# Kernel tuning notes

Hardware: AMD Instinct MI355X
Metric: run time of the kernel (lower is better)

The kernel has to match this reference:

```python
import jax, jax.numpy as jnp
import numpy as np

DIM = 1024
HID = 1536  # int(1024 * 1.5)
K = 4       # conv kernel size
N, T = 4, 4096


def _mk_forget_base(h, a=0.001, b=0.1, lo=-4.323, hi=-9.0):
    x = np.log(np.expm1(np.linspace(a, b, h, dtype=np.float64)))
    x = (x - x.min()) / (x.max() - x.min())
    x = x * abs(hi - lo) + hi
    return jnp.asarray(x, dtype=jnp.float32)


def setup_inputs() -> dict:
    key = jax.random.key(0)
    ks = jax.random.split(key, 6)
    x = jax.random.normal(ks[0], (N, T, DIM), jnp.float32)
    Wi = jax.random.normal(ks[1], (2 * HID, DIM), jnp.float32) * DIM ** -0.5
    conv_w = jax.random.normal(ks[2], (HID, 1, K), jnp.float32) * K ** -0.5
    conv_b = jax.random.normal(ks[3], (HID,), jnp.float32) * 0.01
    Wg = jax.random.normal(ks[4], (2 * HID, HID), jnp.float32) * HID ** -0.5
    bg = jnp.zeros((2 * HID,), jnp.float32)
    forget_base = _mk_forget_base(HID)
    Wo = jax.random.normal(ks[5], (DIM, HID), jnp.float32) * HID ** -0.5
    return {"x": x, "Wi": Wi, "conv_w": conv_w, "conv_b": conv_b,
            "Wg": Wg, "bg": bg, "forget_base": forget_base, "Wo": Wo}


def reference(x, Wi, conv_w, conv_b, Wg, bg, forget_base, Wo):
    # input projection -> gate, x  (each [N,T,HID])
    gi = jnp.einsum('ntc,hc->nth', x, Wi)
    gate, u = jnp.split(gi, 2, axis=-1)
    # causal depthwise conv1d (torch pads k-1 both sides then slices [:T])
    u = jax.lax.conv_general_dilated(
        u.transpose(0, 2, 1),            # [N,HID,T]
        conv_w,                           # [HID,1,K]
        window_strides=(1,),
        padding=[(K - 1, 0)],
        dimension_numbers=('NCH', 'OIH', 'NCH'),
        feature_group_count=HID,
    ) + conv_b[None, :, None]
    u = u.transpose(0, 2, 1)              # [N,T,HID]
    # gates
    fg = jnp.einsum('nth,gh->ntg', u, Wg) + bg
    forget, inp = jnp.split(fg, 2, axis=-1)
    # RG-LRU decay: alpha = exp(-8 * softplus(forget_base) * sigmoid(forget))
    alpha = jnp.exp(-8.0 * jax.nn.softplus(forget_base) * jax.nn.sigmoid(forget))
    beta = jnp.sqrt(1.0 - alpha ** 2 + 1e-6)
    xt = beta * jax.nn.sigmoid(inp) * u
    # linear recurrence h_t = alpha_t * h_{t-1} + x_t
    def step(h, ax):
        a, xx = ax
        h = a * h + xx
        return h, h
    _, h = jax.lax.scan(step, jnp.zeros((x.shape[0], HID), x.dtype),
                        (alpha.transpose(1, 0, 2), xt.transpose(1, 0, 2)))
    h = h.transpose(1, 0, 2)              # [N,T,HID]
    # output projection with exact (erf) gelu gate, matching torch default
    return jnp.einsum('nth,ch->ntc', jax.nn.gelu(gate, approximate=False) * h, Wo)
```

## Files before the change

kernel.cpp:

```cpp
#include <hip/hip_runtime.h>

#define DIM 1024
#define HID 1536
#define TT 4096
#define NB 4
#define KCONV 4
#define MROWS (NB * TT)
#define NC 128
#define CH (TT / NC)
#define H8 (HID / 8)
#define H4 (HID / 4)
#define TC 16

typedef unsigned short u16;
typedef short bf16x8 __attribute__((ext_vector_type(8)));
typedef u16 u16x4 __attribute__((ext_vector_type(4)));
typedef float f32x4 __attribute__((ext_vector_type(4)));

__device__ __forceinline__ u16 f2bf(float f) {
  union { float f; unsigned u; } v; v.f = f;
  unsigned r = (v.u + 0x7fffu + ((v.u >> 16) & 1u)) >> 16;
  return (u16)r;
}
__device__ __forceinline__ float bf2f(u16 h) {
  union { unsigned u; float f; } v; v.u = ((unsigned)h) << 16;
  return v.f;
}
__device__ __forceinline__ float gelu_exact(float g) {
  return 0.5f * g * (1.0f + erff(g * 0.70710678118f));
}

__global__ void cvt_bf16(const float* __restrict__ in, u16* __restrict__ out, int n4) {
  int i = blockIdx.x * blockDim.x + threadIdx.x;
  if (i < n4) {
    float4 v = reinterpret_cast<const float4*>(in)[i];
    ushort4 o;
    o.x = f2bf(v.x); o.y = f2bf(v.y); o.z = f2bf(v.z); o.w = f2bf(v.w);
    reinterpret_cast<ushort4*>(out)[i] = o;
  }
}

#define AS1q __attribute__((address_space(1)))
#define AS3q __attribute__((address_space(3)))
__device__ __forceinline__ void glds16(const u16* g, u16* l) {
  __builtin_amdgcn_global_load_lds((const AS1q void*)g, (AS3q void*)l, 16, 0, 0);
}

#define BAR    asm volatile("s_barrier" ::: "memory")
#define WAITV4 asm volatile("s_waitcnt vmcnt(4)" ::: "memory")
#define WAITV0 asm volatile("s_waitcnt vmcnt(0)" ::: "memory")

template <int EPI>
__global__ __launch_bounds__(512, 2) void gemm256(
    const u16* __restrict__ A, const u16* __restrict__ B,
    float* __restrict__ C, u16* __restrict__ O0, u16* __restrict__ O1,
    int M, int Nn, int K, int gx) {
  __shared__ u16 LA[2][2][8192];
  __shared__ u16 LB[2][2][8192];
  const int tid = threadIdx.x;
  const int l = tid & 63;
  const int wid = tid >> 6;
  const int wr = wid >> 2;
  const int wc = wid & 3;

  const int bid = blockIdx.x;
  const int gm8 = (M >> 8) >> 3;
  const int xcd = bid & 7;
  const int idx = bid >> 3;
  const int mg  = idx / (4 * gx);
  const int rem = idx % (4 * gx);
  const int nn  = rem >> 2;
  const int mi  = rem & 3;
  const int tileM = (xcd * gm8 + mg * 4 + mi) * 256;
  const int tileN = nn * 256;

  const int lp = l ^ ((l & 32) >> 4);
  const int srow = lp >> 2;
  const int scol = (lp & 3) * 8;
  const int rdoff = ((l & 15) * 32 + (l >> 4) * 8) ^ ((l & 8) << 1);

  const u16* Abase = A + (size_t)(tileM + wid * 32 + srow) * K + scol;
  const u16* Bbase = B + (size_t)(tileN + wid * 32 + srow) * K + scol;

#define STAGE_A(c, kk, kt) { const u16* g_ = Abase + (size_t)(kt) * 64 + (kk) * 32; \
    glds16(g_, &LA[c][kk][wid * 1024]); glds16(g_ + 16 * (size_t)K, &LA[c][kk][wid * 1024 + 512]); }
#define STAGE_B(c, kk, kt) { const u16* g_ = Bbase + (size_t)(kt) * 64 + (kk) * 32; \
    glds16(g_, &LB[c][kk][wid * 1024]); glds16(g_ + 16 * (size_t)K, &LB[c][kk][wid * 1024 + 512]); }

  f32x4 acc[8][4] = {};
  bf16x8 a[8], b[4];

#define LDB4(c, kk) { _Pragma("unroll") for (int ni = 0; ni < 4; ni++) \
    b[ni] = *(const bf16x8*)&LB[c][kk][(wc * 4 + ni) * 512 + rdoff]; }
#define LDA8(c, kk) { _Pragma("unroll") for (int mi2 = 0; mi2 < 8; mi2++) \
    a[mi2] = *(const bf16x8*)&LA[c][kk][(wr * 8 + mi2) * 512 + rdoff]; }
#define MFMA32 { __builtin_amdgcn_s_setprio(1); \
    _Pragma("unroll") for (int mi2 = 0; mi2 < 8; mi2++) \
    _Pragma("unroll") for (int ni = 0; ni < 4; ni++) \
      acc[mi2][ni] = __builtin_amdgcn_mfma_f32_16x16x32_bf16(a[mi2], b[ni], acc[mi2][ni], 0, 0, 0); \
    __builtin_amdgcn_s_setprio(0); }

  STAGE_A(0, 0, 0); STAGE_B(0, 0, 0);
  STAGE_A(0, 1, 0); STAGE_B(0, 1, 0);
  STAGE_A(1, 0, 1); STAGE_B(1, 0, 1);
  WAITV4; BAR;

  const int NIT = K >> 7;
  for (int i = 0; i < NIT; i++) {
    const int kt = 2 * i;
    const bool nl = (i + 1 < NIT);
    LDB4(0, 0); LDA8(0, 0); STAGE_A(1, 1, kt + 1); STAGE_B(1, 1, kt + 1);
    BAR; MFMA32; BAR;
    LDB4(0, 1); LDA8(0, 1); if (nl) { STAGE_A(0, 0, kt + 2); STAGE_B(0, 0, kt + 2); }
    BAR; MFMA32; if (nl) { WAITV4; } else { WAITV0; } BAR;
    LDB4(1, 0); LDA8(1, 0); if (nl) { STAGE_A(0, 1, kt + 2); STAGE_B(0, 1, kt + 2); }
    BAR; MFMA32; BAR;
    LDB4(1, 1); LDA8(1, 1); if (nl) { STAGE_A(1, 0, kt + 3); STAGE_B(1, 0, kt + 3); }
    BAR; MFMA32; if (nl) { WAITV4; } else { WAITV0; } BAR;
  }

  const int r0 = tileM + wr * 128 + (l >> 4) * 4;
  const int c0 = tileN + wc * 64 + (l & 15);
  if (EPI == 0) {
#pragma unroll
    for (int ai = 0; ai < 8; ai++)
#pragma unroll
      for (int ni = 0; ni < 4; ni++)
#pragma unroll
        for (int r = 0; r < 4; r++)
          C[(size_t)(r0 + ai * 16 + r) * Nn + (c0 + ni * 16)] = acc[ai][ni][r];
  } else {
    const bool lo = (tileN < HID);
    u16* dst = lo ? O0 : O1;
    const int cb = lo ? 0 : HID;
#pragma unroll
    for (int ai = 0; ai < 8; ai++)
#pragma unroll
      for (int ni = 0; ni < 4; ni++)
#pragma unroll
        for (int r = 0; r < 4; r++) {
          float v = acc[ai][ni][r];
          if (EPI == 2 && lo) v = gelu_exact(v);
          dst[(size_t)(r0 + ai * 16 + r) * HID + (c0 + ni * 16 - cb)] = f2bf(v);
        }
  }
#undef STAGE_A
#undef STAGE_B
#undef LDB4
#undef LDA8
#undef MFMA32
}

__global__ void conv1d_k(const u16* __restrict__ u, const float* __restrict__ w,
                         const float* __restrict__ b, u16* __restrict__ uc) {
  int idx = blockIdx.x * blockDim.x + threadIdx.x;
  int hb = (idx % H8) * 8;
  int rc = idx / H8;
  int t0 = (rc % (TT / TC)) * TC;
  int n  = rc / (TT / TC);

  float wt[KCONV][8], bias[8];
#pragma unroll
  for (int j = 0; j < 8; j++) {
    float4 wj = reinterpret_cast<const float4*>(w)[hb + j];
    wt[0][j] = wj.x; wt[1][j] = wj.y; wt[2][j] = wj.z; wt[3][j] = wj.w;
    bias[j] = b[hb + j];
  }

  const u16* up = u + (size_t)n * TT * HID + hb;
  u16* op = uc + (size_t)n * TT * HID + hb;
  bf16x8 zero;
#pragma unroll
  for (int j = 0; j < 8; j++) zero[j] = 0;
  bf16x8 w0 = (t0 > 0) ? *(const bf16x8*)&up[(size_t)(t0 - 3) * HID] : zero;
  bf16x8 w1 = (t0 > 0) ? *(const bf16x8*)&up[(size_t)(t0 - 2) * HID] : zero;
  bf16x8 w2 = (t0 > 0) ? *(const bf16x8*)&up[(size_t)(t0 - 1) * HID] : zero;
#pragma unroll 4
  for (int t = t0; t < t0 + TC; t++) {
    bf16x8 cur = *(const bf16x8*)&up[(size_t)t * HID];
    bf16x8 o;
#pragma unroll
    for (int j = 0; j < 8; j++) {
      float a = bias[j];
      a += bf2f((u16)w0[j]) * wt[0][j];
      a += bf2f((u16)w1[j]) * wt[1][j];
      a += bf2f((u16)w2[j]) * wt[2][j];
      a += bf2f((u16)cur[j]) * wt[3][j];
      o[j] = (short)f2bf(a);
    }
    *(bf16x8*)&op[(size_t)t * HID] = o;
    w0 = w1; w1 = w2; w2 = cur;
  }
}

__global__ void scan_phase1(const u16* __restrict__ fbuf, const u16* __restrict__ ibuf,
                            const u16* __restrict__ ubuf, const float* __restrict__ fb,
                            const float* __restrict__ bg,
                            float* __restrict__ Ac, float* __restrict__ Bc) {
  int tid = blockIdx.x * blockDim.x + threadIdx.x;
  int hb = (tid % H4) * 4;
  int nc = tid / H4;
  int n = nc % NB;
  int c = nc / NB;
  f32x4 fbv = *reinterpret_cast<const f32x4*>(&fb[hb]);
  f32x4 bgf = *reinterpret_cast<const f32x4*>(&bg[hb]);
  f32x4 bgi = *reinterpret_cast<const f32x4*>(&bg[HID + hb]);
  float c8[4], ap[4] = {1.f, 1.f, 1.f, 1.f}, hl[4] = {0.f, 0.f, 0.f, 0.f};
#pragma unroll
  for (int j = 0; j < 4; j++) c8[j] = 8.0f * log1pf(expf(fbv[j]));
  size_t base = ((size_t)n * TT + (size_t)c * CH) * HID + hb;
  for (int t = 0; t < CH; t++) {
    size_t ix = base + (size_t)t * HID;
    u16x4 f4 = *reinterpret_cast<const u16x4*>(&fbuf[ix]);
    u16x4 i4 = *reinterpret_cast<const u16x4*>(&ibuf[ix]);
    u16x4 u4 = *reinterpret_cast<const u16x4*>(&ubuf[ix]);
#pragma unroll
    for (int j = 0; j < 4; j++) {
      float f = bf2f(f4[j]) + bgf[j];
      float sf = 1.0f / (1.0f + expf(-f));
      float al = expf(-c8[j] * sf);
      float be = sqrtf(1.0f - al * al + 1e-6f);
      float xi = bf2f(i4[j]) + bgi[j];
      float si = 1.0f / (1.0f + expf(-xi));
      float xt = be * si * bf2f(u4[j]);
      hl[j] = al * hl[j] + xt;
      ap[j] *= al;
    }
  }
  size_t ci = ((size_t)c * NB + n) * HID + hb;
  *reinterpret_cast<f32x4*>(&Ac[ci]) = f32x4{ap[0], ap[1], ap[2], ap[3]};
  *reinterpret_cast<f32x4*>(&Bc[ci]) = f32x4{hl[0], hl[1], hl[2], hl[3]};
}

__global__ void scan_phase2(const float* __restrict__ Ac, const float* __restrict__ Bc,
                            float* __restrict__ Carry) {
  int tid = blockIdx.x * blockDim.x + threadIdx.x;
  int h = tid % HID;
  int n = tid / HID;
  float carry = 0.f;
#pragma unroll 4
  for (int c = 0; c < NC; c++) {
    size_t ci = ((size_t)c * NB + n) * HID + h;
    Carry[ci] = carry;
    carry = Ac[ci] * carry + Bc[ci];
  }
}

__global__ void scan_phase3(const u16* __restrict__ fbuf, const u16* __restrict__ ibuf,
                            const u16* __restrict__ ubuf, const u16* __restrict__ gbuf,
                            const float* __restrict__ fb, const float* __restrict__ bg,
                            const float* __restrict__ Carry, u16* __restrict__ gh) {
  int tid = blockIdx.x * blockDim.x + threadIdx.x;
  int hb = (tid % H4) * 4;
  int nc = tid / H4;
  int n = nc % NB;
  int c = nc / NB;
  f32x4 fbv = *reinterpret_cast<const f32x4*>(&fb[hb]);
  f32x4 bgf = *reinterpret_cast<const f32x4*>(&bg[hb]);
  f32x4 bgi = *reinterpret_cast<const f32x4*>(&bg[HID + hb]);
  float c8[4], hc[4];
#pragma unroll
  for (int j = 0; j < 4; j++) c8[j] = 8.0f * log1pf(expf(fbv[j]));
  size_t ci = ((size_t)c * NB + n) * HID + hb;
  f32x4 cv = *reinterpret_cast<const f32x4*>(&Carry[ci]);
#pragma unroll
  for (int j = 0; j < 4; j++) hc[j] = cv[j];
  size_t base = ((size_t)n * TT + (size_t)c * CH) * HID + hb;
  for (int t = 0; t < CH; t++) {
    size_t ix = base + (size_t)t * HID;
    u16x4 f4 = *reinterpret_cast<const u16x4*>(&fbuf[ix]);
    u16x4 i4 = *reinterpret_cast<const u16x4*>(&ibuf[ix]);
    u16x4 u4 = *reinterpret_cast<const u16x4*>(&ubuf[ix]);
    u16x4 g4 = *reinterpret_cast<const u16x4*>(&gbuf[ix]);
    u16x4 o4;
#pragma unroll
    for (int j = 0; j < 4; j++) {
      float f = bf2f(f4[j]) + bgf[j];
      float sf = 1.0f / (1.0f + expf(-f));
      float al = expf(-c8[j] * sf);
      float be = sqrtf(1.0f - al * al + 1e-6f);
      float xi = bf2f(i4[j]) + bgi[j];
      float si = 1.0f / (1.0f + expf(-xi));
      float xt = be * si * bf2f(u4[j]);
      hc[j] = al * hc[j] + xt;
      o4[j] = f2bf(bf2f(g4[j]) * hc[j]);
    }
    *reinterpret_cast<u16x4*>(&gh[ix]) = o4;
  }
}

extern "C" void kernel_launch(void* const* d_in, const int* in_sizes, int n_in,
                              void* d_out, int out_size, void* d_ws, size_t ws_size,
                              hipStream_t stream) {
  const float* x  = (const float*)d_in[0];
  const float* Wi = (const float*)d_in[1];
  const float* cw = (const float*)d_in[2];
  const float* cb = (const float*)d_in[3];
  const float* Wg = (const float*)d_in[4];
  const float* bg = (const float*)d_in[5];
  const float* fb = (const float*)d_in[6];
  const float* Wo = (const float*)d_in[7];
  float* out = (float*)d_out;

  const size_t SZ_XBF = (size_t)MROWS * DIM * 2;
  const size_t SZ_WI  = (size_t)2 * HID * DIM * 2;
  const size_t SZ_WG  = (size_t)2 * HID * HID * 2;
  const size_t SZ_WO  = (size_t)DIM * HID * 2;
  const size_t SZ_ACT = (size_t)MROWS * HID * 2;
  const size_t REQUIRED = SZ_XBF + SZ_WI + SZ_WG + SZ_WO + 4 * SZ_ACT;
  if (ws_size < REQUIRED) return;

  char* p = (char*)d_ws;
  auto alloc = [&](size_t bytes) { char* q = p; p += bytes; return q; };
  u16* x_bf   = (u16*)alloc(SZ_XBF);
  u16* Wi_bf  = (u16*)alloc(SZ_WI);
  u16* Wg_bf  = (u16*)alloc(SZ_WG);
  u16* Wo_bf  = (u16*)alloc(SZ_WO);
  u16* u_bf   = (u16*)alloc(SZ_ACT);
  u16* uc_bf  = (u16*)alloc(SZ_ACT);
  u16* fg0_bf = (u16*)alloc(SZ_ACT);
  u16* fg1_bf = (u16*)alloc(SZ_ACT);
  u16* gh_bf  = u_bf;

  u16* gate_bf = (u16*)d_out;
  float* Ac    = (float*)((char*)d_out + SZ_ACT);
  float* Bc    = Ac + (size_t)NC * NB * HID;
  float* Carry = Bc + (size_t)NC * NB * HID;

  cvt_bf16<<<(MROWS * DIM / 4) / 256, 256, 0, stream>>>(x, x_bf, MROWS * DIM / 4);
  cvt_bf16<<<(2 * HID * DIM / 4) / 256, 256, 0, stream>>>(Wi, Wi_bf, 2 * HID * DIM / 4);
  cvt_bf16<<<(2 * HID * HID / 4) / 256, 256, 0, stream>>>(Wg, Wg_bf, 2 * HID * HID / 4);
  cvt_bf16<<<(DIM * HID / 4) / 256, 256, 0, stream>>>(Wo, Wo_bf, DIM * HID / 4);

  gemm256<2><<<(2 * HID / 256) * (MROWS / 256), 512, 0, stream>>>(
      x_bf, Wi_bf, nullptr, gate_bf, u_bf, MROWS, 2 * HID, DIM, 2 * HID / 256);
  conv1d_k<<<(NB * (TT / TC) * H8) / 256, 256, 0, stream>>>(u_bf, cw, cb, uc_bf);
  gemm256<1><<<(2 * HID / 256) * (MROWS / 256), 512, 0, stream>>>(
      uc_bf, Wg_bf, nullptr, fg0_bf, fg1_bf, MROWS, 2 * HID, HID, 2 * HID / 256);
  scan_phase1<<<(NB * H4 * NC) / 256, 256, 0, stream>>>(fg0_bf, fg1_bf, uc_bf, fb, bg, Ac, Bc);
  scan_phase2<<<(NB * HID) / 64, 64, 0, stream>>>(Ac, Bc, Carry);
  scan_phase3<<<(NB * H4 * NC) / 256, 256, 0, stream>>>(fg0_bf, fg1_bf, uc_bf, gate_bf, fb, bg, Carry, gh_bf);
  gemm256<0><<<(DIM / 256) * (MROWS / 256), 512, 0, stream>>>(
      gh_bf, Wo_bf, out, nullptr, nullptr, MROWS, DIM, HID, DIM / 256);
}
```

Baseline: 576.9 us.

## Stage GEMM epilogue through LDS for vectorized stores; move prefetch after MFMA

The GEMM epilogue now writes accumulator fragments into shared memory in row chunks, then reads them back as full rows and writes them to global memory with 16-byte vector stores. This replaces the scattered scalar stores of 4-byte floats or 2-byte bf16 values. The main loop also issues the global-to-LDS staging loads after each MFMA block instead of before it, which shifts when memory traffic overlaps with compute. In exchange the epilogue gains extra barriers and LDS round trips, and the reordered staging may expose more load latency.

```diff
diff --git a/kernel.cpp b/kernel.cpp
--- a/kernel.cpp
+++ b/kernel.cpp
@@ -109,40 +109,69 @@
   for (int i = 0; i < NIT; i++) {
     const int kt = 2 * i;
     const bool nl = (i + 1 < NIT);
-    LDB4(0, 0); LDA8(0, 0); STAGE_A(1, 1, kt + 1); STAGE_B(1, 1, kt + 1);
-    BAR; MFMA32; BAR;
-    LDB4(0, 1); LDA8(0, 1); if (nl) { STAGE_A(0, 0, kt + 2); STAGE_B(0, 0, kt + 2); }
-    BAR; MFMA32; if (nl) { WAITV4; } else { WAITV0; } BAR;
-    LDB4(1, 0); LDA8(1, 0); if (nl) { STAGE_A(0, 1, kt + 2); STAGE_B(0, 1, kt + 2); }
-    BAR; MFMA32; BAR;
-    LDB4(1, 1); LDA8(1, 1); if (nl) { STAGE_A(1, 0, kt + 3); STAGE_B(1, 0, kt + 3); }
-    BAR; MFMA32; if (nl) { WAITV4; } else { WAITV0; } BAR;
-  }
-
-  const int r0 = tileM + wr * 128 + (l >> 4) * 4;
-  const int c0 = tileN + wc * 64 + (l & 15);
+    LDB4(0, 0); LDA8(0, 0);
+    BAR; MFMA32; STAGE_A(1, 1, kt + 1); STAGE_B(1, 1, kt + 1); BAR;
+    LDB4(0, 1); LDA8(0, 1);
+    BAR; MFMA32; if (nl) { STAGE_A(0, 0, kt + 2); STAGE_B(0, 0, kt + 2); WAITV4; } else { WAITV0; } BAR;
+    LDB4(1, 0); LDA8(1, 0);
+    BAR; MFMA32; if (nl) { STAGE_A(0, 1, kt + 2); STAGE_B(0, 1, kt + 2); } BAR;
+    LDB4(1, 1); LDA8(1, 1);
+    BAR; MFMA32; if (nl) { STAGE_A(1, 0, kt + 3); STAGE_B(1, 0, kt + 3); WAITV4; } else { WAITV0; } BAR;
+  }
+
   if (EPI == 0) {
-#pragma unroll
-    for (int ai = 0; ai < 8; ai++)
-#pragma unroll
-      for (int ni = 0; ni < 4; ni++)
-#pragma unroll
-        for (int r = 0; r < 4; r++)
-          C[(size_t)(r0 + ai * 16 + r) * Nn + (c0 + ni * 16)] = acc[ai][ni][r];
+    float* Lf = (float*)&LA[0][0][0];
+#pragma unroll
+    for (int ch = 0; ch < 8; ch++) {
+      const int wrh = ch >> 2, ab = (ch & 3) * 2;
+      if (wr == wrh) {
+#pragma unroll
+        for (int a2 = 0; a2 < 2; a2++)
+#pragma unroll
+          for (int ni = 0; ni < 4; ni++)
+#pragma unroll
+            for (int r = 0; r < 4; r++)
+              Lf[((l >> 4) * 4 + a2 * 16 + r) * 256 + wc * 64 + ni * 16 + (l & 15)] =
+                  acc[ab + a2][ni][r];
+      }
+      BAR;
+      const int row = tid >> 4, co = (tid & 15) * 16;
+#pragma unroll
+      for (int q = 0; q < 4; q++) {
+        float4 v = *(const float4*)&Lf[row * 256 + co + q * 4];
+        *(float4*)&C[(size_t)(tileM + ch * 32 + row) * Nn + (tileN + co + q * 4)] = v;
+      }
+      BAR;
+    }
   } else {
+    u16* Ls = (u16*)&LA[0][0][0];
     const bool lo = (tileN < HID);
     u16* dst = lo ? O0 : O1;
     const int cb = lo ? 0 : HID;
 #pragma unroll
-    for (int ai = 0; ai < 8; ai++)
-#pragma unroll
-      for (int ni = 0; ni < 4; ni++)
-#pragma unroll
-        for (int r = 0; r < 4; r++) {
-          float v = acc[ai][ni][r];
-          if (EPI == 2 && lo) v = gelu_exact(v);
-          dst[(size_t)(r0 + ai * 16 + r) * HID + (c0 + ni * 16 - cb)] = f2bf(v);
-        }
+    for (int ch = 0; ch < 4; ch++) {
+      const int wrh = ch >> 1, ab = (ch & 1) * 4;
+      if (wr == wrh) {
+#pragma unroll
+        for (int a2 = 0; a2 < 4; a2++)
+#pragma unroll
+          for (int ni = 0; ni < 4; ni++)
+#pragma unroll
+            for (int r = 0; r < 4; r++) {
+              float v = acc[ab + a2][ni][r];
+              if (EPI == 2 && lo) v = gelu_exact(v);
+              Ls[((l >> 4) * 4 + a2 * 16 + r) * 256 + wc * 64 + ni * 16 + (l & 15)] = f2bf(v);
+            }
+      }
+      BAR;
+      const int row = tid >> 3, co = (tid & 7) * 32;
+#pragma unroll
+      for (int q = 0; q < 4; q++) {
+        bf16x8 v = *(const bf16x8*)&Ls[row * 256 + co + q * 8];
+        *(bf16x8*)&dst[(size_t)(tileM + ch * 64 + row) * HID + (tileN + co + q * 8 - cb)] = v;
+      }
+      BAR;
+    }
   }
 #undef STAGE_A
 #undef STAGE_B
```

Measured after the change: 677.1 us. +17.4%, slower.
